# Kernel optimization log

Hardware: AMD Instinct MI355X
Metric: run time of the kernel (lower is better)

The kernel has to match this reference:

```python
import jax, jax.numpy as jnp
import numpy as np

FORGET_BIAS = 1.0  # tf.nn.rnn_cell.LSTMCell default
HIDDEN = 64


def setup_inputs() -> dict:
    key = jax.random.key(0)
    k1, k2 = jax.random.split(key)
    B, T, D = 4096, 9, 512
    x = jax.random.normal(k1, (B, T, D), dtype=jnp.float32)
    # Fused LSTM kernel: [(D + H), 4H], gate order (i, j, f, o) as in TF LSTMCell
    kernel = jax.random.normal(k2, (D + HIDDEN, 4 * HIDDEN), dtype=jnp.float32) * 0.02
    bias = jnp.zeros((4 * HIDDEN,), dtype=jnp.float32)
    return {"x": x, "kernel": kernel, "bias": bias}


def _lstm_scan(x, kernel, bias):
    B, T, D = x.shape
    H = HIDDEN
    # Split kernel into input and recurrent parts for a cleaner scan body.
    Wx = kernel[:D]          # [D, 4H]
    Wh = kernel[D:]          # [H, 4H]
    # Precompute input contributions for all timesteps in one big GEMM.
    xg = jnp.einsum('btd,dg->btg', x, Wx) + bias  # [B, T, 4H]

    def step(carry, xg_t):
        c, h = carry
        gates = xg_t + h @ Wh  # [B, 4H]
        i, j, f, o = jnp.split(gates, 4, axis=-1)  # TF gate order: i, j, f, o
        c_new = jax.nn.sigmoid(f + FORGET_BIAS) * c + jax.nn.sigmoid(i) * jnp.tanh(j)
        h_new = jax.nn.sigmoid(o) * jnp.tanh(c_new)
        return (c_new, h_new), h_new

    c0 = jnp.zeros((B, H), dtype=x.dtype)
    h0 = jnp.zeros((B, H), dtype=x.dtype)
    _, hs = jax.lax.scan(step, (c0, h0), jnp.swapaxes(xg, 0, 1))  # hs: [T, B, H]
    return jnp.transpose(hs, (1, 0, 2))  # [B, T, H]


def reference(x, kernel, bias):
    return _lstm_scan(x, kernel, bias)
```

## Files before the change

### kernel.cpp

```cpp
#include <hip/hip_runtime.h>
#include <math.h>

#define T_STEPS 9
#define D_IN    512
#define HID     64
#define G4      256
#define BPB     8
#define NCH     8

typedef short  short8 __attribute__((ext_vector_type(8)));
typedef float  f32x4  __attribute__((ext_vector_type(4)));
typedef unsigned int uint;
typedef unsigned short ushort;

__device__ __forceinline__ ushort f2bf(float f) {
    uint u = __float_as_uint(f);
    u = (u + 0x7FFFu + ((u >> 16) & 1u)) >> 16;
    return (ushort)u;
}
__device__ __forceinline__ float fsig(float x) {
    return 1.0f / (1.0f + __expf(-x));
}
__device__ __forceinline__ float ftanh(float x) {
    float t = __expf(-2.0f * fabsf(x));
    float r = (1.0f - t) / (1.0f + t);
    return copysignf(r, x);
}
__device__ __forceinline__ uint cvtpk(float a, float b) {
    uint r;
    asm("v_cvt_pk_bf16_f32 %0, %1, %2" : "=v"(r) : "v"(a), "v"(b));
    return r;
}

__global__ __launch_bounds__(256)
void prep_w(const float* __restrict__ kern, ushort* __restrict__ wxT,
            ushort* __restrict__ whT)
{
    const int blk = blockIdx.x;
    const int n   = threadIdx.x;
    const int krow0 = (blk < 64) ? blk * 8 : 512 + (blk - 64) * 8;
    union { ushort us[8]; short8 v; } o;
    #pragma unroll
    for (int j = 0; j < 8; ++j)
        o.us[j] = f2bf(kern[(size_t)(krow0 + j) * G4 + n]);
    if (blk < 64) *(short8*)&wxT[((size_t)blk * 256 + n) * 8] = o.v;
    else          *(short8*)&whT[((size_t)(blk - 64) * 256 + n) * 8] = o.v;
}

__global__ __launch_bounds__(256, 2)
void lstm_fused(const float* __restrict__ x, const ushort* __restrict__ wxT,
                const ushort* __restrict__ whT, const float* __restrict__ bias,
                float* __restrict__ out)
{
    __shared__ __align__(16) ushort sA[3][80 * 64];
    __shared__ __align__(16) ushort sH[1024];

    const int t = threadIdx.x;
    const int w = t >> 6, l = t & 63;
    const int lane15 = l & 15, quad = l >> 4;
    const int u = w * 16 + lane15;

    const float* xbase = x + (size_t)blockIdx.x * (72 * D_IN);
    const int sq = t & 15, ow = sq >> 1, hw = sq & 1;
    int src[5], wad[5];
    #pragma unroll
    for (int j = 0; j < 5; ++j) {
        int row = j * 16 + (t >> 4);
        int b_ = row & 7, s_ = row >> 3;
        if (s_ > 8) s_ = 8;
        src[j] = (b_ * 9 + s_) * 512 + sq * 4;
        wad[j] = row * 64 + ((ow ^ (row & 7)) << 3) + (hw << 2);
    }

    if (t < 128) {
        uint4 z = {0u, 0u, 0u, 0u};
        *(uint4*)&sH[t * 8] = z;
    }

    float4 svA[5], svB[5];
    #pragma unroll
    for (int j = 0; j < 5; ++j) svA[j] = *(const float4*)&xbase[src[j]];
    #pragma unroll
    for (int j = 0; j < 5; ++j) svB[j] = *(const float4*)&xbase[src[j] + 64];

    short8 bFb[2][2][4];
    #pragma unroll
    for (int kk = 0; kk < 2; ++kk)
        #pragma unroll
        for (int g = 0; g < 4; ++g)
            bFb[0][kk][g] = *(const short8*)
                &wxT[(size_t)((kk * 4 + quad) * 256 + g * 64 + u) * 8];

    #pragma unroll
    for (int j = 0; j < 5; ++j) {
        uint2 p;
        p.x = cvtpk(svA[j].x, svA[j].y);
        p.y = cvtpk(svA[j].z, svA[j].w);
        *(uint2*)&sA[0][wad[j]] = p;
    }
    #pragma unroll
    for (int j = 0; j < 5; ++j) svA[j] = *(const float4*)&xbase[src[j] + 128];

    f32x4 acc[5][4];
    #pragma unroll
    for (int i = 0; i < 5; ++i)
        #pragma unroll
        for (int g = 0; g < 4; ++g)
            acc[i][g] = (f32x4){0.f, 0.f, 0.f, 0.f};

    #pragma unroll
    for (int k = 0; k < NCH; ++k) {
        if (k < NCH - 1) {
            #pragma unroll
            for (int j = 0; j < 5; ++j) {
                float4 v = ((k + 1) & 1) ? svB[j] : svA[j];
                uint2 p;
                p.x = cvtpk(v.x, v.y);
                p.y = cvtpk(v.z, v.w);
                *(uint2*)&sA[(k + 1) % 3][wad[j]] = p;
            }
        }
        if (k < NCH - 1) {
            #pragma unroll
            for (int kk = 0; kk < 2; ++kk)
                #pragma unroll
                for (int g = 0; g < 4; ++g)
                    bFb[(k + 1) & 1][kk][g] = *(const short8*)
                        &wxT[(size_t)((((k + 1) * 2 + kk) * 4 + quad) * 256
                                      + g * 64 + u) * 8];
        }
        if (k < NCH - 3) {
            #pragma unroll
            for (int j = 0; j < 5; ++j) {
                float4 v = *(const float4*)&xbase[src[j] + (k + 3) * 64];
                if ((k + 3) & 1) svB[j] = v; else svA[j] = v;
            }
        }
        asm volatile("s_waitcnt lgkmcnt(0)" ::: "memory");
        __builtin_amdgcn_sched_barrier(0);
        __builtin_amdgcn_s_barrier();
        __builtin_amdgcn_sched_barrier(0);
        asm volatile("" ::: "memory");
        #pragma unroll
        for (int kk = 0; kk < 2; ++kk) {
            #pragma unroll
            for (int i = 0; i < 5; ++i) {
                int row = i * 16 + lane15;
                short8 aF = *(const short8*)
                    &sA[k % 3][row * 64 + (((kk * 4 + quad) ^ (row & 7)) << 3)];
                #pragma unroll
                for (int g = 0; g < 4; ++g)
                    acc[i][g] = __builtin_amdgcn_mfma_f32_16x16x32_bf16(
                        aF, bFb[k & 1][kk][g], acc[i][g], 0, 0, 0);
            }
        }
    }

    short8 whF[4][2];
    #pragma unroll
    for (int g = 0; g < 4; ++g)
        #pragma unroll
        for (int kh = 0; kh < 2; ++kh)
            whF[g][kh] = *(const short8*)
                &whT[(size_t)((kh * 4 + quad) * 256 + g * 64 + u) * 8];

    float bia[4];
    bia[0] = bias[u];
    bia[1] = bias[64 + u];
    bia[2] = bias[128 + u] + 1.0f;
    bia[3] = bias[192 + u];

    float cst[4] = {0.f, 0.f, 0.f, 0.f};
    const int b0 = blockIdx.x * BPB;

    #pragma unroll
    for (int s = 0; s < T_STEPS; ++s) {
        const int  i = s >> 1;
        const int  p = s & 1;
        const bool active = ((quad >> 1) == p);
        const int  bofs = (quad & 1) * 4;

        f32x4 g4[4];
        #pragma unroll
        for (int g = 0; g < 4; ++g)
            #pragma unroll
            for (int r = 0; r < 4; ++r)
                g4[g][r] = acc[i][g][r] + bia[g];

        short8 aF[2];
        #pragma unroll
        for (int kh = 0; kh < 2; ++kh)
            aF[kh] = *(const short8*)&sH[((kh * 4 + quad) * 16 + lane15) * 8];

        #pragma unroll
        for (int g = 0; g < 4; ++g)
            #pragma unroll
            for (int kh = 0; kh < 2; ++kh)
                g4[g] = __builtin_amdgcn_mfma_f32_16x16x32_bf16(
                    aF[kh], whF[g][kh], g4[g], 0, 0, 0);

        const int wrow = 8 * ((s + 1) & 1);
        #pragma unroll
        for (int r = 0; r < 4; ++r) {
            float cp = __shfl_xor(cst[r], 32);
            if (active) {
                float ii = fsig(g4[0][r]);
                float jj = ftanh(g4[1][r]);
                float ff = fsig(g4[2][r]);
                float oo = fsig(g4[3][r]);
                float c  = ff * cp + ii * jj;
                cst[r] = c;
                float h = oo * ftanh(c);
                int bb = bofs + r;
                out[((size_t)(b0 + bb) * T_STEPS + s) * HID + u] = h;
                sH[((u >> 3) * 16 + wrow + bb) * 8 + (u & 7)] = f2bf(h);
            }
        }
        asm volatile("s_waitcnt lgkmcnt(0)" ::: "memory");
        __builtin_amdgcn_sched_barrier(0);
        __builtin_amdgcn_s_barrier();
        __builtin_amdgcn_sched_barrier(0);
    }
}

extern "C" void kernel_launch(void* const* d_in, const int* in_sizes, int n_in,
                              void* d_out, int out_size, void* d_ws, size_t ws_size,
                              hipStream_t stream)
{
    const float* x    = (const float*)d_in[0];
    const float* kern = (const float*)d_in[1];
    const float* bias = (const float*)d_in[2];
    float* out = (float*)d_out;

    const int B = in_sizes[0] / (T_STEPS * D_IN);

    ushort* wxT = (ushort*)d_ws;
    ushort* whT = (ushort*)((char*)d_ws + 262144);

    prep_w<<<72, 256, 0, stream>>>(kern, wxT, whT);
    lstm_fused<<<B / BPB, 256, 0, stream>>>(x, wxT, whT, bias, out);
}
```

Baseline: 127.1 us.

## Halve batch rows per block to four and raise occupancy to three blocks

Each workgroup now handles 4 batch rows instead of 8. That shrinks the input tile to 48 padded rows and the accumulators to 3 M-tiles, doubles the grid size, and raises the launch-bounds occupancy hint to 3 blocks per CU. The recurrent phase now rotates the active quad across four timesteps, and the cell state moves between quads with a rotate-by-48 shuffle instead of an xor-32 shuffle. Weight fragments are no longer double-buffered; they are loaded at the start of each chunk, which saves registers but exposes that load latency. The recurrence also wastes more MFMA work, since the 16-row tile carries only 4 useful rows, and the Wx weights are re-read twice as often across blocks.

```diff
diff --git a/kernel.cpp b/kernel.cpp
--- a/kernel.cpp
+++ b/kernel.cpp
@@ -5,7 +5,8 @@
 #define D_IN    512
 #define HID     64
 #define G4      256
-#define BPB     8
+#define BPB     4
+#define MROWS   48
 #define NCH     8
 
 typedef short  short8 __attribute__((ext_vector_type(8)));
@@ -47,12 +48,12 @@
     else          *(short8*)&whT[((size_t)(blk - 64) * 256 + n) * 8] = o.v;
 }
 
-__global__ __launch_bounds__(256, 2)
+__global__ __launch_bounds__(256, 3)
 void lstm_fused(const float* __restrict__ x, const ushort* __restrict__ wxT,
                 const ushort* __restrict__ whT, const float* __restrict__ bias,
                 float* __restrict__ out)
 {
-    __shared__ __align__(16) ushort sA[3][80 * 64];
+    __shared__ __align__(16) ushort sA[3][MROWS * 64];
     __shared__ __align__(16) ushort sH[1024];
 
     const int t = threadIdx.x;
@@ -60,13 +61,13 @@
     const int lane15 = l & 15, quad = l >> 4;
     const int u = w * 16 + lane15;
 
-    const float* xbase = x + (size_t)blockIdx.x * (72 * D_IN);
+    const float* xbase = x + (size_t)blockIdx.x * (BPB * T_STEPS * D_IN);
     const int sq = t & 15, ow = sq >> 1, hw = sq & 1;
-    int src[5], wad[5];
-    #pragma unroll
-    for (int j = 0; j < 5; ++j) {
+    int src[3], wad[3];
+    #pragma unroll
+    for (int j = 0; j < 3; ++j) {
         int row = j * 16 + (t >> 4);
-        int b_ = row & 7, s_ = row >> 3;
+        int b_ = row & 3, s_ = row >> 2;
         if (s_ > 8) s_ = 8;
         src[j] = (b_ * 9 + s_) * 512 + sq * 4;
         wad[j] = row * 64 + ((ow ^ (row & 7)) << 3) + (hw << 2);
@@ -77,42 +78,40 @@
         *(uint4*)&sH[t * 8] = z;
     }
 
-    float4 svA[5], svB[5];
-    #pragma unroll
-    for (int j = 0; j < 5; ++j) svA[j] = *(const float4*)&xbase[src[j]];
-    #pragma unroll
-    for (int j = 0; j < 5; ++j) svB[j] = *(const float4*)&xbase[src[j] + 64];
-
-    short8 bFb[2][2][4];
-    #pragma unroll
-    for (int kk = 0; kk < 2; ++kk)
-        #pragma unroll
-        for (int g = 0; g < 4; ++g)
-            bFb[0][kk][g] = *(const short8*)
-                &wxT[(size_t)((kk * 4 + quad) * 256 + g * 64 + u) * 8];
-
-    #pragma unroll
-    for (int j = 0; j < 5; ++j) {
+    float4 svA[3], svB[3];
+    #pragma unroll
+    for (int j = 0; j < 3; ++j) svA[j] = *(const float4*)&xbase[src[j]];
+    #pragma unroll
+    for (int j = 0; j < 3; ++j) svB[j] = *(const float4*)&xbase[src[j] + 64];
+    #pragma unroll
+    for (int j = 0; j < 3; ++j) {
         uint2 p;
         p.x = cvtpk(svA[j].x, svA[j].y);
         p.y = cvtpk(svA[j].z, svA[j].w);
         *(uint2*)&sA[0][wad[j]] = p;
     }
     #pragma unroll
-    for (int j = 0; j < 5; ++j) svA[j] = *(const float4*)&xbase[src[j] + 128];
-
-    f32x4 acc[5][4];
-    #pragma unroll
-    for (int i = 0; i < 5; ++i)
+    for (int j = 0; j < 3; ++j) svA[j] = *(const float4*)&xbase[src[j] + 128];
+
+    f32x4 acc[3][4];
+    #pragma unroll
+    for (int i = 0; i < 3; ++i)
         #pragma unroll
         for (int g = 0; g < 4; ++g)
             acc[i][g] = (f32x4){0.f, 0.f, 0.f, 0.f};
 
     #pragma unroll
     for (int k = 0; k < NCH; ++k) {
+        short8 bFb[2][4];
+        #pragma unroll
+        for (int kk = 0; kk < 2; ++kk)
+            #pragma unroll
+            for (int g = 0; g < 4; ++g)
+                bFb[kk][g] = *(const short8*)
+                    &wxT[(size_t)(((k * 2 + kk) * 4 + quad) * 256 + g * 64 + u) * 8];
         if (k < NCH - 1) {
             #pragma unroll
-            for (int j = 0; j < 5; ++j) {
+            for (int j = 0; j < 3; ++j) {
                 float4 v = ((k + 1) & 1) ? svB[j] : svA[j];
                 uint2 p;
                 p.x = cvtpk(v.x, v.y);
@@ -120,18 +119,9 @@
                 *(uint2*)&sA[(k + 1) % 3][wad[j]] = p;
             }
         }
-        if (k < NCH - 1) {
-            #pragma unroll
-            for (int kk = 0; kk < 2; ++kk)
-                #pragma unroll
-                for (int g = 0; g < 4; ++g)
-                    bFb[(k + 1) & 1][kk][g] = *(const short8*)
-                        &wxT[(size_t)((((k + 1) * 2 + kk) * 4 + quad) * 256
-                                      + g * 64 + u) * 8];
-        }
         if (k < NCH - 3) {
             #pragma unroll
-            for (int j = 0; j < 5; ++j) {
+            for (int j = 0; j < 3; ++j) {
                 float4 v = *(const float4*)&xbase[src[j] + (k + 3) * 64];
                 if ((k + 3) & 1) svB[j] = v; else svA[j] = v;
             }
@@ -140,18 +130,17 @@
         __builtin_amdgcn_sched_barrier(0);
         __builtin_amdgcn_s_barrier();
         __builtin_amdgcn_sched_barrier(0);
-        asm volatile("" ::: "memory");
         #pragma unroll
         for (int kk = 0; kk < 2; ++kk) {
             #pragma unroll
-            for (int i = 0; i < 5; ++i) {
+            for (int i = 0; i < 3; ++i) {
                 int row = i * 16 + lane15;
                 short8 aF = *(const short8*)
                     &sA[k % 3][row * 64 + (((kk * 4 + quad) ^ (row & 7)) << 3)];
                 #pragma unroll
                 for (int g = 0; g < 4; ++g)
                     acc[i][g] = __builtin_amdgcn_mfma_f32_16x16x32_bf16(
-                        aF, bFb[k & 1][kk][g], acc[i][g], 0, 0, 0);
+                        aF, bFb[kk][g], acc[i][g], 0, 0, 0);
             }
         }
     }
@@ -175,11 +164,8 @@
 
     #pragma unroll
     for (int s = 0; s < T_STEPS; ++s) {
-        const int  i = s >> 1;
-        const int  p = s & 1;
-        const bool active = ((quad >> 1) == p);
-        const int  bofs = (quad & 1) * 4;
-
+        const int  i = s >> 2;
+        const bool active = (quad == (s & 3));
         f32x4 g4[4];
         #pragma unroll
         for (int g = 0; g < 4; ++g)
@@ -199,10 +185,10 @@
                 g4[g] = __builtin_amdgcn_mfma_f32_16x16x32_bf16(
                     aF[kh], whF[g][kh], g4[g], 0, 0, 0);
 
-        const int wrow = 8 * ((s + 1) & 1);
+        const int wrow = ((s + 1) & 3) * 4;
         #pragma unroll
         for (int r = 0; r < 4; ++r) {
-            float cp = __shfl_xor(cst[r], 32);
+            float cp = __shfl(cst[r], (l + 48) & 63);
             if (active) {
                 float ii = fsig(g4[0][r]);
                 float jj = ftanh(g4[1][r]);
@@ -211,9 +197,8 @@
                 float c  = ff * cp + ii * jj;
                 cst[r] = c;
                 float h = oo * ftanh(c);
-                int bb = bofs + r;
-                out[((size_t)(b0 + bb) * T_STEPS + s) * HID + u] = h;
-                sH[((u >> 3) * 16 + wrow + bb) * 8 + (u & 7)] = f2bf(h);
+                out[((size_t)(b0 + r) * T_STEPS + s) * HID + u] = h;
+                sH[((u >> 3) * 16 + wrow + r) * 8 + (u & 7)] = f2bf(h);
             }
         }
         asm volatile("s_waitcnt lgkmcnt(0)" ::: "memory");
```

Measured after the change: 140.3 us. 10.4% more time.
